# Performance work log

Measured on AMD Instinct MI355X. Metric: run time of the kernel, lower is better.

The kernel has to match this reference:

```python
import jax, jax.numpy as jnp
import numpy as np

ALPHA = 0.5
MOM = 0.9            # momentum m in the recurrence
ACTIVATION = "tanh"
NUM_LAYERS = 2
CACHE = 32           # GROUP size
NK = 4               # n_kernel_feats
B, N, E = 4, 4096, 128


def _act(T):
    if ACTIVATION == "leaky-relu":
        return jax.nn.leaky_relu(T)
    elif ACTIVATION == "tanh":
        return jnp.tanh(T)
    return T


def _group_indices(N, cache, stage):
    # vectorized group_pos_to_index_v2 over all (group_nr, pos_in_group)
    m = N // cache
    o = np.arange(cache)
    s = 0 if stage == 0 else (1 << (stage - 1)) % m
    g = np.arange(m)[:, None]
    block = (g + o[None, :] * s) % m
    return jnp.asarray(block * cache + o[None, :])  # [m, cache], a permutation of 0..N-1


def _ncn_layer(X, Xa, W, stage):
    B, N, E = X.shape
    ce = E // NK
    m = N // CACHE
    idx = _group_indices(N, CACHE, stage)           # [m, cache]
    Wi = W[:E].reshape(NK, ce)
    Wj = W[E:].reshape(NK, ce)
    # gather groups: [B, m, NK, cache, ce]
    xg = jnp.moveaxis(X.reshape(B, N, NK, ce)[:, idx], 3, 2)
    xag = jnp.moveaxis(Xa.reshape(B, N, NK, ce)[:, idx], 3, 2)

    def step(carry, j):
        xi, xa = carry                               # [B, m, NK, cache, ce]
        xj = jnp.take(xi, j, axis=3)                 # [B, m, NK, ce]  (row start_j)
        sim = (jnp.einsum('bgnke,ne->bgnk', xi, Wi)
               + jnp.einsum('bgne,ne->bgn', xj, Wj)[..., None])   # [B, m, NK, cache]
        T = ALPHA * xi + (1.0 - ALPHA) * sim[..., None] * xj[:, :, :, None, :]
        F = _act(T)
        ya = MOM * xa + (1.0 - MOM) * F
        yi = MOM * xi + (1.0 - MOM) * ya
        return (yi, ya), None

    (yi, ya), _ = jax.lax.scan(step, (xg, xag), jnp.arange(CACHE))

    # scatter back; idx is a permutation so .set reproduces the += into zeros
    def scatter(v):
        v = jnp.moveaxis(v, 2, 3).reshape(B, m * CACHE, E)
        return jnp.zeros((B, N, E), v.dtype).at[:, idx.reshape(-1)].set(v)

    return scatter(yi), scatter(ya)


def setup_inputs() -> dict:
    key = jax.random.key(0)
    k1, k2, k3 = jax.random.split(key, 3)
    x = jax.random.normal(k1, (B, N, E), jnp.float32)
    xa = jax.random.normal(k2, (B, N, E), jnp.float32)
    W = jax.random.normal(k3, (NUM_LAYERS, 2 * E), jnp.float32)
    return {"x": x, "xa": xa, "W": W}


def reference(x, xa, W):
    for l in range(NUM_LAYERS):
        x, xa = _ncn_layer(x, xa, W[l], l)
    return x, xa
```

## Files before the change

kernel.cpp:

```cpp
#include <hip/hip_runtime.h>


namespace {
constexpr int kB = 4;
constexpr int kN = 4096;
constexpr int kE = 128;
constexpr int kCE = 32;
constexpr int kCache = 32;
constexpr int kM = kN / kCache;

constexpr float kL1    = 1.4426950408889634f;
constexpr float kInvL1 = 0.6931471805599453f;

typedef __attribute__((ext_vector_type(2))) float f32x2;

__device__ __forceinline__ f32x2 pk_fma(f32x2 a, f32x2 b, f32x2 c) {
    return __builtin_elementwise_fma(a, b, c);
}

__device__ __forceinline__ float pair_sum(float x) {
    int sw = __builtin_amdgcn_update_dpp(0, __float_as_int(x),
                                         0xB1, 0xF, 0xF, true);
    return x + __int_as_float(sw);
}

__device__ __forceinline__ f32x2 bperm2(int byte_addr, f32x2 v) {
    f32x2 r;
    r.x = __int_as_float(
        __builtin_amdgcn_ds_bpermute(byte_addr, __float_as_int(v.x)));
    r.y = __int_as_float(
        __builtin_amdgcn_ds_bpermute(byte_addr, __float_as_int(v.y)));
    return r;
}
}

__global__ void __launch_bounds__(256, 2) ncn_layer_kernel(
    const float* __restrict__ x_in, const float* __restrict__ xa_in,
    const float* __restrict__ Wl,
    float* __restrict__ x_out, float* __restrict__ xa_out,
    int s)
{
    const int t    = threadIdx.x;
    const int wv   = t >> 6;
    const int l    = t & 63;
    const int unit = blockIdx.x * 4 + wv;
    const int n    = unit & 3;
    const int g    = (unit >> 2) & (kM - 1);
    const int b    = unit >> 9;

    const int h = l & 1;
    const int r = l >> 1;

    const int gr = (((g + r * s) & (kM - 1)) << 5) + r;
    const size_t base = ((size_t)(b * kN + gr)) * kE + n * kCE + h * 16;

    f32x2 xi[8], ya[8], wi[8], wj[8];
    {
        const float4* xi4 = reinterpret_cast<const float4*>(x_in + base);
        const float4* xa4 = reinterpret_cast<const float4*>(xa_in + base);
        const float4* wi4 = reinterpret_cast<const float4*>(Wl + n * kCE + h * 16);
        const float4* wj4 = reinterpret_cast<const float4*>(Wl + kE + n * kCE + h * 16);
#pragma unroll
        for (int q4 = 0; q4 < 4; ++q4) {
            float4 v = xi4[q4];
            xi[2 * q4 + 0] = f32x2{v.x * kL1, v.y * kL1};
            xi[2 * q4 + 1] = f32x2{v.z * kL1, v.w * kL1};
            float4 a = xa4[q4];
            ya[2 * q4 + 0] = f32x2{a.x * (0.1f * kL1), a.y * (0.1f * kL1)};
            ya[2 * q4 + 1] = f32x2{a.z * (0.1f * kL1), a.w * (0.1f * kL1)};
            float4 u = wi4[q4];
            wi[2 * q4 + 0] = f32x2{u.x * kInvL1, u.y * kInvL1};
            wi[2 * q4 + 1] = f32x2{u.z * kInvL1, u.w * kInvL1};
            float4 w2 = wj4[q4];
            wj[2 * q4 + 0] = f32x2{w2.x * kInvL1, w2.y * kInvL1};
            wj[2 * q4 + 1] = f32x2{w2.z * kInvL1, w2.w * kInvL1};
        }
    }

    const int v4h = h << 2;

    const f32x2 one = {1.0f, 1.0f};
    const f32x2 c9  = {0.9f, 0.9f};
    const f32x2 cA  = {0.01f * kL1, 0.01f * kL1};
    const f32x2 cB  = {-0.02f * kL1, -0.02f * kL1};

#pragma unroll
    for (int j = 0; j < kCache; ++j) {
        const int addr = v4h + 8 * j;
        f32x2 xj[8];
#pragma unroll
        for (int q = 0; q < 8; ++q) xj[q] = bperm2(addr, xi[q]);

        f32x2 a0 = xi[0] * wi[0], a1 = xi[1] * wi[1];
        f32x2 e0 = xi[0] * wj[0], e1 = xi[1] * wj[1];
        a0 = pk_fma(xi[2], wi[2], a0); a1 = pk_fma(xi[3], wi[3], a1);
        e0 = pk_fma(xi[2], wj[2], e0); e1 = pk_fma(xi[3], wj[3], e1);
        a0 = pk_fma(xi[4], wi[4], a0); a1 = pk_fma(xi[5], wi[5], a1);
        e0 = pk_fma(xi[4], wj[4], e0); e1 = pk_fma(xi[5], wj[5], e1);
        a0 = pk_fma(xi[6], wi[6], a0); a1 = pk_fma(xi[7], wi[7], a1);
        e0 = pk_fma(xi[6], wj[6], e0); e1 = pk_fma(xi[7], wj[7], e1);
        f32x2 av = a0 + a1, ev = e0 + e1;
        float a = av.x + av.y;
        float e = ev.x + ev.y;
        a = pair_sum(a);
        e = pair_sum(e);

        const float dj = __int_as_float(
            __builtin_amdgcn_readlane(__float_as_int(e), 2 * j));
        const float sim = a + dj;
        const f32x2 sv = {sim, sim};

#pragma unroll
        for (int q = 0; q < 8; ++q) {
            f32x2 arg = pk_fma(xj[q], sv, xi[q]);
            f32x2 t2;
            t2.x = __builtin_amdgcn_exp2f(arg.x);
            t2.y = __builtin_amdgcn_exp2f(arg.y);
            f32x2 den = t2 + one;
            f32x2 rc;
            rc.x = __builtin_amdgcn_rcpf(den.x);
            rc.y = __builtin_amdgcn_rcpf(den.y);
            f32x2 yt = pk_fma(ya[q], c9, cA);
            ya[q] = pk_fma(rc, cB, yt);
            xi[q] = pk_fma(xi[q], c9, ya[q]);
        }
    }

    {
        const f32x2 ivx = {kInvL1, kInvL1};
        const f32x2 iva = {10.0f * kInvL1, 10.0f * kInvL1};
        float4* xo4 = reinterpret_cast<float4*>(x_out + base);
        float4* ao4 = reinterpret_cast<float4*>(xa_out + base);
#pragma unroll
        for (int q4 = 0; q4 < 4; ++q4) {
            f32x2 x0 = xi[2 * q4 + 0] * ivx;
            f32x2 x1 = xi[2 * q4 + 1] * ivx;
            float4 v; v.x = x0.x; v.y = x0.y; v.z = x1.x; v.w = x1.y;
            xo4[q4] = v;
            f32x2 a0 = ya[2 * q4 + 0] * iva;
            f32x2 a1 = ya[2 * q4 + 1] * iva;
            float4 w; w.x = a0.x; w.y = a0.y; w.z = a1.x; w.w = a1.y;
            ao4[q4] = w;
        }
    }
}

extern "C" void kernel_launch(void* const* d_in, const int* in_sizes, int n_in,
                              void* d_out, int out_size, void* d_ws, size_t ws_size,
                              hipStream_t stream) {
    const float* x  = (const float*)d_in[0];
    const float* xa = (const float*)d_in[1];
    const float* W  = (const float*)d_in[2];

    const size_t plane = (size_t)kB * kN * kE;

    float* x_mid  = (float*)d_ws;
    float* xa_mid = x_mid + plane;

    float* x_out  = (float*)d_out;
    float* xa_out = x_out + plane;

    const dim3 grid(kB * kM);
    const dim3 block(256);

    ncn_layer_kernel<<<grid, block, 0, stream>>>(x, xa, W, x_mid, xa_mid, 0);
    ncn_layer_kernel<<<grid, block, 0, stream>>>(x_mid, xa_mid, W + 2 * kE,
                                                 x_out, xa_out, 1);
}
```

Measured before the change: 119.2 us.

## Fuse both NCN layers into one cooperative kernel with a grid sync

Replaces the two per-layer launches with a single cooperative kernel that runs layer 0, then a grid-wide barrier, then layer 1. Layer 1 reads and writes the output buffers in place instead of going through a workspace. The intermediate stays in the internally scaled domain, so the rescale on layer 0 output and on layer 1 input is skipped. The aim is to remove the second launch and the inter-kernel gap. In exchange it adds the grid-sync cost and relies on all 512 blocks being co-resident.

Measured after the change: 247.5 us. 108% more time.

```diff
diff --git a/kernel.cpp b/kernel.cpp
--- a/kernel.cpp
+++ b/kernel.cpp
@@ -1,4 +1,5 @@
 #include <hip/hip_runtime.h>
+#include <hip/hip_cooperative_groups.h>
 
 
 namespace {
@@ -32,26 +33,20 @@
         __builtin_amdgcn_ds_bpermute(byte_addr, __float_as_int(v.y)));
     return r;
 }
-}
 
-__global__ void __launch_bounds__(256, 2) ncn_layer_kernel(
-    const float* __restrict__ x_in, const float* __restrict__ xa_in,
-    const float* __restrict__ Wl,
-    float* __restrict__ x_out, float* __restrict__ xa_out,
-    int s)
+template <int S, bool IN_SCALED, bool OUT_SCALED>
+__device__ __forceinline__ void ncn_layer(
+    const float* x_in, const float* xa_in, const float* Wl,
+    float* x_out, float* xa_out, int unit, int l)
 {
-    const int t    = threadIdx.x;
-    const int wv   = t >> 6;
-    const int l    = t & 63;
-    const int unit = blockIdx.x * 4 + wv;
-    const int n    = unit & 3;
-    const int g    = (unit >> 2) & (kM - 1);
-    const int b    = unit >> 9;
+    const int n = unit & 3;
+    const int g = (unit >> 2) & (kM - 1);
+    const int b = unit >> 9;
 
     const int h = l & 1;
     const int r = l >> 1;
 
-    const int gr = (((g + r * s) & (kM - 1)) << 5) + r;
+    const int gr = (((g + r * S) & (kM - 1)) << 5) + r;
     const size_t base = ((size_t)(b * kN + gr)) * kE + n * kCE + h * 16;
 
     f32x2 xi[8], ya[8], wi[8], wj[8];
@@ -63,11 +58,18 @@
 #pragma unroll
         for (int q4 = 0; q4 < 4; ++q4) {
             float4 v = xi4[q4];
-            xi[2 * q4 + 0] = f32x2{v.x * kL1, v.y * kL1};
-            xi[2 * q4 + 1] = f32x2{v.z * kL1, v.w * kL1};
             float4 a = xa4[q4];
-            ya[2 * q4 + 0] = f32x2{a.x * (0.1f * kL1), a.y * (0.1f * kL1)};
-            ya[2 * q4 + 1] = f32x2{a.z * (0.1f * kL1), a.w * (0.1f * kL1)};
+            if constexpr (IN_SCALED) {
+                xi[2 * q4 + 0] = f32x2{v.x, v.y};
+                xi[2 * q4 + 1] = f32x2{v.z, v.w};
+                ya[2 * q4 + 0] = f32x2{a.x, a.y};
+                ya[2 * q4 + 1] = f32x2{a.z, a.w};
+            } else {
+                xi[2 * q4 + 0] = f32x2{v.x * kL1, v.y * kL1};
+                xi[2 * q4 + 1] = f32x2{v.z * kL1, v.w * kL1};
+                ya[2 * q4 + 0] = f32x2{a.x * (0.1f * kL1), a.y * (0.1f * kL1)};
+                ya[2 * q4 + 1] = f32x2{a.z * (0.1f * kL1), a.w * (0.1f * kL1)};
+            }
             float4 u = wi4[q4];
             wi[2 * q4 + 0] = f32x2{u.x * kInvL1, u.y * kInvL1};
             wi[2 * q4 + 1] = f32x2{u.z * kInvL1, u.w * kInvL1};
@@ -127,22 +129,42 @@
     }
 
     {
-        const f32x2 ivx = {kInvL1, kInvL1};
-        const f32x2 iva = {10.0f * kInvL1, 10.0f * kInvL1};
         float4* xo4 = reinterpret_cast<float4*>(x_out + base);
         float4* ao4 = reinterpret_cast<float4*>(xa_out + base);
 #pragma unroll
         for (int q4 = 0; q4 < 4; ++q4) {
-            f32x2 x0 = xi[2 * q4 + 0] * ivx;
-            f32x2 x1 = xi[2 * q4 + 1] * ivx;
+            f32x2 x0 = xi[2 * q4 + 0], x1 = xi[2 * q4 + 1];
+            f32x2 a0 = ya[2 * q4 + 0], a1 = ya[2 * q4 + 1];
+            if constexpr (!OUT_SCALED) {
+                const f32x2 ivx = {kInvL1, kInvL1};
+                const f32x2 iva = {10.0f * kInvL1, 10.0f * kInvL1};
+                x0 = x0 * ivx; x1 = x1 * ivx;
+                a0 = a0 * iva; a1 = a1 * iva;
+            }
             float4 v; v.x = x0.x; v.y = x0.y; v.z = x1.x; v.w = x1.y;
             xo4[q4] = v;
-            f32x2 a0 = ya[2 * q4 + 0] * iva;
-            f32x2 a1 = ya[2 * q4 + 1] * iva;
             float4 w; w.x = a0.x; w.y = a0.y; w.z = a1.x; w.w = a1.y;
             ao4[q4] = w;
         }
     }
+}
+}
+
+__global__ void __launch_bounds__(256, 2) ncn_fused_kernel(
+    const float* __restrict__ x, const float* __restrict__ xa,
+    const float* __restrict__ W,
+    float* __restrict__ xo, float* __restrict__ ao)
+{
+    const int t = threadIdx.x;
+    const int unit = blockIdx.x * 4 + (t >> 6);
+    const int l = t & 63;
+
+    ncn_layer<0, false, true>(x, xa, W, xo, ao, unit, l);
+
+    __threadfence();
+    cooperative_groups::this_grid().sync();
+
+    ncn_layer<1, true, false>(xo, ao, W + 2 * kE, xo, ao, unit, l);
 }
 
 extern "C" void kernel_launch(void* const* d_in, const int* in_sizes, int n_in,
@@ -154,16 +176,11 @@
 
     const size_t plane = (size_t)kB * kN * kE;
 
-    float* x_mid  = (float*)d_ws;
-    float* xa_mid = x_mid + plane;
-
     float* x_out  = (float*)d_out;
     float* xa_out = x_out + plane;
 
-    const dim3 grid(kB * kM);
-    const dim3 block(256);
-
-    ncn_layer_kernel<<<grid, block, 0, stream>>>(x, xa, W, x_mid, xa_mid, 0);
-    ncn_layer_kernel<<<grid, block, 0, stream>>>(x_mid, xa_mid, W + 2 * kE,
-                                                 x_out, xa_out, 1);
+    void* args[5] = {(void*)&x, (void*)&xa, (void*)&W,
+                     (void*)&x_out, (void*)&xa_out};
+    hipLaunchCooperativeKernel((const void*)ncn_fused_kernel,
+                               dim3(kB * kM), dim3(256), args, 0, stream);
 }
```
